# Optimization experiments

Hardware: AMD Instinct MI355X
Metric: run time of the kernel (lower is better)

Reference implementation:

```python
import jax, jax.numpy as jnp
import numpy as np

# Model dims (mamba_ssm defaults for d_model=256)
IN_DIM = 64
D_MODEL = 256
D_INNER = 512      # expand=2
D_STATE = 16
D_CONV = 4
DT_RANK = 16       # ceil(d_model/16)
N_LAYERS = 4
BATCH = 8
SEQ = 1024


def setup_inputs() -> dict:
    key = jax.random.key(0)
    ks = jax.random.split(key, 10)
    s = lambda k, shape, sc: jax.random.normal(k, shape, jnp.float32) * sc
    return {
        "x": jax.random.normal(ks[0], (BATCH, SEQ, IN_DIM), jnp.float32),
        "Wp": s(ks[1], (D_MODEL, IN_DIM), 0.1),
        "bp": jnp.zeros((D_MODEL,), jnp.float32),
        "W_in": s(ks[2], (N_LAYERS, 2 * D_INNER, D_MODEL), 0.05),
        "conv_w": s(ks[3], (N_LAYERS, D_INNER, D_CONV), 0.2),
        "conv_b": jnp.zeros((N_LAYERS, D_INNER), jnp.float32),
        "W_x": s(ks[4], (N_LAYERS, DT_RANK + 2 * D_STATE, D_INNER), 0.05),
        "W_dt": s(ks[5], (N_LAYERS, D_INNER, DT_RANK), 0.1),
        "b_dt": jnp.full((N_LAYERS, D_INNER), -4.6, jnp.float32),  # softplus -> dt ~ 0.01
        "A_log": jnp.log(jnp.broadcast_to(
            jnp.arange(1, D_STATE + 1, dtype=jnp.float32), (N_LAYERS, D_INNER, D_STATE))),
        "Dp": jnp.ones((N_LAYERS, D_INNER), jnp.float32),
        "W_out": s(ks[6], (N_LAYERS, D_MODEL, D_INNER), 0.05),
        "ln_g": jnp.ones((N_LAYERS, D_MODEL), jnp.float32),
        "ln_b": jnp.zeros((N_LAYERS, D_MODEL), jnp.float32),
        "Wf": s(ks[7], (1, D_MODEL), 0.1),
        "bf": jnp.zeros((1,), jnp.float32),
    }


def _layernorm(x, g, b):
    m = x.mean(-1, keepdims=True)
    v = x.var(-1, keepdims=True)
    return (x - m) * jax.lax.rsqrt(v + 1e-5) * g + b


def _mamba(x, W_in, cw, cb, W_x, W_dt, b_dt, A_log, Dp, W_out):
    B, L, _ = x.shape
    xz = jnp.einsum('bld,ed->ble', x, W_in)          # (B,L,2*D_INNER)
    xh, z = jnp.split(xz, 2, axis=-1)
    # causal depthwise conv1d (kernel D_CONV) + silu
    xp = jnp.pad(xh, ((0, 0), (D_CONV - 1, 0), (0, 0)))
    xc = sum(xp[:, k:k + L, :] * cw[:, k] for k in range(D_CONV)) + cb
    xc = jax.nn.silu(xc)
    # input-dependent dt, B, C
    x_dbl = jnp.einsum('bld,ed->ble', xc, W_x)
    dtr = x_dbl[..., :DT_RANK]
    Bm = x_dbl[..., DT_RANK:DT_RANK + D_STATE]       # (B,L,N)
    Cm = x_dbl[..., -D_STATE:]                       # (B,L,N)
    dt = jax.nn.softplus(jnp.einsum('blr,dr->bld', dtr, W_dt) + b_dt)
    A = -jnp.exp(A_log)                              # (D,N)
    dA = jnp.exp(dt[..., None] * A)                  # (B,L,D,N)
    dBu = dt[..., None] * Bm[:, :, None, :] * xc[..., None]
    def step(h, inp):
        dA_t, dBu_t, C_t = inp
        h = dA_t * h + dBu_t                         # (B,D,N)
        return h, jnp.einsum('bdn,bn->bd', h, C_t)
    h0 = jnp.zeros((B, D_INNER, D_STATE), x.dtype)
    _, ys = jax.lax.scan(step, h0, (dA.transpose(1, 0, 2, 3),
                                    dBu.transpose(1, 0, 2, 3),
                                    Cm.transpose(1, 0, 2)))
    y = ys.transpose(1, 0, 2) + Dp * xc              # (B,L,D)
    y = y * jax.nn.silu(z)
    return jnp.einsum('ble,de->bld', y, W_out)


def reference(x, Wp, bp, W_in, conv_w, conv_b, W_x, W_dt, b_dt, A_log, Dp, W_out, ln_g, ln_b, Wf, bf):
    h = jnp.einsum('bli,di->bld', x, Wp) + bp
    for l in range(N_LAYERS):
        y = _mamba(h, W_in[l], conv_w[l], conv_b[l], W_x[l], W_dt[l],
                   b_dt[l], A_log[l], Dp[l], W_out[l])
        h = _layernorm(y, ln_g[l], ln_b[l])          # dropout is identity at eval
    pooled = h.mean(axis=1)                          # AdaptiveAvgPool1d(1) over L
    return pooled @ Wf.T + bf
```

## Files before the change

kernel.cpp:

```cpp
#include <hip/hip_runtime.h>
#include <hip/hip_bf16.h>
#include <math.h>

#define SEQ_LEN 1024
#define BATCH_N 8
#define DMODEL 256
#define DINNER 512
#define DSTATE 16
#define DTRANK 16
#define ROWS (BATCH_N * SEQ_LEN)
#define NCHUNK 64
#define CHUNK (SEQ_LEN / NCHUNK)
#define BD 8

typedef unsigned short u16;
typedef u16 u16x8 __attribute__((ext_vector_type(8)));
typedef short bf16x8 __attribute__((ext_vector_type(8)));
typedef float f32x4 __attribute__((ext_vector_type(4)));

__device__ __forceinline__ float siluf(float x) { return x / (1.f + expf(-x)); }
__device__ __forceinline__ float softplusf(float x) {
    return fmaxf(x, 0.f) + log1pf(expf(-fabsf(x)));
}
__device__ __forceinline__ float fexpf(float x) { return __expf(x); }
__device__ __forceinline__ float softplus_fast(float x) {
    return fmaxf(x, 0.f) + __logf(1.f + __expf(-fabsf(x)));
}
__device__ __forceinline__ float silu_fast(float x) {
    return x * __builtin_amdgcn_rcpf(1.f + __expf(-x));
}
__device__ __forceinline__ u16 bf16_rne(float x) {
    unsigned u = __builtin_bit_cast(unsigned, x);
    return (u16)((u + 0x7FFFu + ((u >> 16) & 1u)) >> 16);
}
__device__ __forceinline__ void cvt_hl(float x, u16& h, u16& l) {
    unsigned u = __builtin_bit_cast(unsigned, x);
    unsigned hb = (u + 0x7FFFu + ((u >> 16) & 1u)) >> 16;
    h = (u16)hb;
    float hf = __builtin_bit_cast(float, hb << 16);
    l = bf16_rne(x - hf);
}
__device__ __forceinline__ float pair_f(u16 h, u16 l) {
    return __builtin_bit_cast(float, (unsigned)h << 16) +
           __builtin_bit_cast(float, (unsigned)l << 16);
}
__device__ __forceinline__ size_t swa(int R, int row, int c) {
    return ((size_t)(c >> 5) * R + row) * 32 + (c & 31);
}

__global__ __launch_bounds__(256) void cvt_x_swz(
    const float* __restrict__ x, u16* __restrict__ dh, u16* __restrict__ dl)
{
    int i = blockIdx.x * 256 + threadIdx.x;
    int row = i >> 6, c = i & 63;
    u16 h, l;
    cvt_hl(x[i], h, l);
    size_t sw = swa(ROWS, row, c);
    dh[sw] = h;
    dl[sw] = l;
}

#define CWT (16384 + 4 * 262144 + 4 * 32768 + 4 * 131072)
__global__ __launch_bounds__(256) void cvt_w_swz(
    const float* __restrict__ Wp, const float* __restrict__ W_in,
    const float* __restrict__ W_x, const float* __restrict__ W_out,
    u16* __restrict__ Wpb, u16* __restrict__ Wib,
    u16* __restrict__ Wxb, u16* __restrict__ Wob)
{
    long i = (long)blockIdx.x * 256 + threadIdx.x;
    if (i >= CWT) return;
    if (i < 16384) {
        int n = (int)(i >> 6), k = (int)(i & 63);
        Wpb[((k >> 5) * 256 + n) * 32 + (k & 31)] = bf16_rne(Wp[n * 64 + k]);
        return;
    }
    i -= 16384;
    if (i < 4 * 262144) {
        int l = (int)(i >> 18), r = (int)(i & 262143);
        int n = r >> 8, k = r & 255;
        Wib[l * 262144 + ((k >> 5) * 1024 + n) * 32 + (k & 31)] =
            bf16_rne(W_in[l * 262144 + n * 256 + k]);
        return;
    }
    i -= 4 * 262144;
    if (i < 4 * 32768) {
        int l = (int)(i >> 15), r = (int)(i & 32767);
        int n = r >> 9, k = r & 511;
        float v = (n < 48) ? W_x[l * 48 * 512 + n * 512 + k] : 0.f;
        Wxb[l * 32768 + ((k >> 5) * 64 + n) * 32 + (k & 31)] = bf16_rne(v);
        return;
    }
    i -= 4 * 32768;
    {
        int l = (int)(i >> 17), r = (int)(i & 131071);
        int n = r >> 9, k = r & 511;
        Wob[l * 131072 + ((k >> 5) * 256 + n) * 32 + (k & 31)] =
            bf16_rne(W_out[l * 131072 + n * 512 + k]);
    }
}

template<int EPI>
__global__ __launch_bounds__(256) void gemm_sw(
    const u16* __restrict__ Ah, const u16* __restrict__ Al,
    const u16* __restrict__ B,
    const float* __restrict__ bias, float* __restrict__ C,
    u16* __restrict__ Ch, u16* __restrict__ Cl,
    int M, int N, int Npad, int K, int ldc)
{
    const int tid  = threadIdx.x;
    const int wave = tid >> 6, lane = tid & 63;
    const int bm   = blockIdx.y * 64, bn = blockIdx.x * 64;
    const int wm   = (wave >> 1) * 32, wn = (wave & 1) * 32;
    const int fr   = lane & 15, quad = lane >> 4;

    f32x4 acc[2][2];
#pragma unroll
    for (int i = 0; i < 2; i++)
#pragma unroll
        for (int j = 0; j < 2; j++) acc[i][j] = (f32x4){0.f, 0.f, 0.f, 0.f};

    const size_t a0 = (size_t)(bm + wm + fr) * 32 + quad * 8;
    const size_t a1 = a0 + 16 * 32;
    const size_t b0 = (size_t)(bn + wn + fr) * 32 + quad * 8;
    const size_t b1 = b0 + 16 * 32;
    const size_t astep = (size_t)M * 32;
    const size_t bstep = (size_t)Npad * 32;

    const u16* pah = Ah;
    const u16* pal = Al;
    const u16* pb  = B;
#pragma unroll 2
    for (int k0 = 0; k0 < K; k0 += 32) {
        bf16x8 ah0 = *(const bf16x8*)(pah + a0);
        bf16x8 ah1 = *(const bf16x8*)(pah + a1);
        bf16x8 al0 = *(const bf16x8*)(pal + a0);
        bf16x8 al1 = *(const bf16x8*)(pal + a1);
        bf16x8 bv0 = *(const bf16x8*)(pb + b0);
        bf16x8 bv1 = *(const bf16x8*)(pb + b1);
        acc[0][0] = __builtin_amdgcn_mfma_f32_16x16x32_bf16(ah0, bv0, acc[0][0], 0, 0, 0);
        acc[0][0] = __builtin_amdgcn_mfma_f32_16x16x32_bf16(al0, bv0, acc[0][0], 0, 0, 0);
        acc[0][1] = __builtin_amdgcn_mfma_f32_16x16x32_bf16(ah0, bv1, acc[0][1], 0, 0, 0);
        acc[0][1] = __builtin_amdgcn_mfma_f32_16x16x32_bf16(al0, bv1, acc[0][1], 0, 0, 0);
        acc[1][0] = __builtin_amdgcn_mfma_f32_16x16x32_bf16(ah1, bv0, acc[1][0], 0, 0, 0);
        acc[1][0] = __builtin_amdgcn_mfma_f32_16x16x32_bf16(al1, bv0, acc[1][0], 0, 0, 0);
        acc[1][1] = __builtin_amdgcn_mfma_f32_16x16x32_bf16(ah1, bv1, acc[1][1], 0, 0, 0);
        acc[1][1] = __builtin_amdgcn_mfma_f32_16x16x32_bf16(al1, bv1, acc[1][1], 0, 0, 0);
        pah += astep; pal += astep; pb += bstep;
    }

#pragma unroll
    for (int i = 0; i < 2; i++) {
        const int r0 = bm + wm + 16 * i + quad * 4;
#pragma unroll
        for (int reg = 0; reg < 4; reg++) {
            const int row = r0 + reg;
#pragma unroll
            for (int j = 0; j < 2; j++) {
                const int col = bn + wn + 16 * j + fr;
                if (col < N) {
                    float v = acc[i][j][reg];
                    if (bias) v += bias[col];
                    if (EPI == 0) {
                        C[(size_t)row * ldc + col] = v;
                    } else {
                        u16 h, l;
                        cvt_hl(v, h, l);
                        size_t sw = swa(M, row, col);
                        Ch[sw] = h;
                        Cl[sw] = l;
                    }
                }
            }
        }
    }
}

__global__ __launch_bounds__(256) void gemm_sw128(
    const u16* __restrict__ Ah, const u16* __restrict__ Al,
    const u16* __restrict__ B, float* __restrict__ C,
    int M, int Npad, int K, int ldc)
{
    const int tid  = threadIdx.x;
    const int wave = tid >> 6, lane = tid & 63;
    const int bm   = blockIdx.y * 64, bn = blockIdx.x * 128;
    const int wm   = (wave >> 1) * 32, wn = (wave & 1) * 64;
    const int fr   = lane & 15, quad = lane >> 4;

    f32x4 acc[2][4];
#pragma unroll
    for (int i = 0; i < 2; i++)
#pragma unroll
        for (int j = 0; j < 4; j++) acc[i][j] = (f32x4){0.f, 0.f, 0.f, 0.f};

    const size_t a0 = (size_t)(bm + wm + fr) * 32 + quad * 8;
    const size_t a1 = a0 + 16 * 32;
    size_t bofs[4];
#pragma unroll
    for (int j = 0; j < 4; j++)
        bofs[j] = (size_t)(bn + wn + 16 * j + fr) * 32 + quad * 8;
    const size_t astep = (size_t)M * 32;
    const size_t bstep = (size_t)Npad * 32;

    const u16* pah = Ah;
    const u16* pal = Al;
    const u16* pb  = B;
    for (int k0 = 0; k0 < K; k0 += 32) {
        bf16x8 ah0 = *(const bf16x8*)(pah + a0);
        bf16x8 ah1 = *(const bf16x8*)(pah + a1);
        bf16x8 al0 = *(const bf16x8*)(pal + a0);
        bf16x8 al1 = *(const bf16x8*)(pal + a1);
        bf16x8 bv[4];
#pragma unroll
        for (int j = 0; j < 4; j++) bv[j] = *(const bf16x8*)(pb + bofs[j]);
#pragma unroll
        for (int j = 0; j < 4; j++) {
            acc[0][j] = __builtin_amdgcn_mfma_f32_16x16x32_bf16(ah0, bv[j], acc[0][j], 0, 0, 0);
            acc[0][j] = __builtin_amdgcn_mfma_f32_16x16x32_bf16(al0, bv[j], acc[0][j], 0, 0, 0);
            acc[1][j] = __builtin_amdgcn_mfma_f32_16x16x32_bf16(ah1, bv[j], acc[1][j], 0, 0, 0);
            acc[1][j] = __builtin_amdgcn_mfma_f32_16x16x32_bf16(al1, bv[j], acc[1][j], 0, 0, 0);
        }
        pah += astep; pal += astep; pb += bstep;
    }

#pragma unroll
    for (int i = 0; i < 2; i++) {
        const int r0 = bm + wm + 16 * i + quad * 4;
#pragma unroll
        for (int reg = 0; reg < 4; reg++) {
            float* crow = C + (size_t)(r0 + reg) * ldc;
#pragma unroll
            for (int j = 0; j < 4; j++)
                crow[bn + wn + 16 * j + fr] = acc[i][j][reg];
        }
    }
}

__global__ __launch_bounds__(256) void conv_silu_k(
    const float* __restrict__ xz, const float* __restrict__ cw,
    const float* __restrict__ cb, u16* __restrict__ xch, u16* __restrict__ xcl)
{
    int idx = blockIdx.x * 256 + threadIdx.x;
    int d = idx & (DINNER - 1);
    int row = idx >> 9;
    int t = row & (SEQ_LEN - 1);
    float4 w = *(const float4*)(cw + d * 4);
    float acc = cb[d];
    const float* p = xz + (size_t)row * 1024 + d;
    if (t >= 3) acc = fmaf(p[-3 * 1024], w.x, acc);
    if (t >= 2) acc = fmaf(p[-2 * 1024], w.y, acc);
    if (t >= 1) acc = fmaf(p[-1 * 1024], w.z, acc);
    acc = fmaf(p[0], w.w, acc);
    float v = siluf(acc);
    u16 h, l;
    cvt_hl(v, h, l);
    size_t sw = swa(ROWS, row, d);
    xch[sw] = h;
    xcl[sw] = l;
}

__global__ __launch_bounds__(512, 4) void scan_k(
    u16* __restrict__ xch,
    u16* __restrict__ xcl,
    const float* __restrict__ xdbl,
    const float* __restrict__ xz,
    const float* __restrict__ A_log,
    const float* __restrict__ Dp,
    const float* __restrict__ Wdt,
    const float* __restrict__ bdt)
{
    const int tid = threadIdx.x;
    const int dl  = tid & (BD - 1);
    const int ch  = tid >> 3;
    const int b   = blockIdx.x & 7;
    const int dg  = blockIdx.x >> 3;
    const int d   = dg * BD + dl;

    __shared__ float ldsS[NCHUNK * BD * 16];
    __shared__ float ldsD[CHUNK * 512];
    __shared__ float ldsT[NCHUNK * BD];

    float wv[16];
#pragma unroll
    for (int i = 0; i < 16; i += 4) *(float4*)&wv[i] = *(const float4*)(Wdt + d * 16 + i);
    const float bb = bdt[d];

    bool pow_ok = true;
#pragma unroll
    for (int n = 0; n < 16; n++) {
        float An = -expf(A_log[d * 16 + n]);
        pow_ok = pow_ok && (fabsf(An + (float)(n + 1)) <= 1e-3f * (float)(n + 1));
    }
    const int t0 = b * SEQ_LEN + ch * CHUNK;
    const int base = (ch * BD + dl) * 16;
    const size_t xcb = ((size_t)(d >> 5) * ROWS) * 32 + (d & 31);

    float S[16];
#pragma unroll
    for (int n = 0; n < 16; n++) S[n] = 0.f;
    float sdt = 0.f;
#pragma unroll 2
    for (int t = 0; t < CHUNK; ++t) {
        const size_t row = (size_t)(t0 + t);
        const float* xr = xdbl + row * 48;
        float qv[16], Bv[16];
#pragma unroll
        for (int i = 0; i < 16; i += 4) *(float4*)&qv[i] = *(const float4*)(xr + i);
#pragma unroll
        for (int i = 0; i < 16; i += 4) *(float4*)&Bv[i] = *(const float4*)(xr + 16 + i);
        float xcv = pair_f(xch[xcb + row * 32], xcl[xcb + row * 32]);
        float s8[8];
#pragma unroll
        for (int i = 0; i < 8; i++) s8[i] = fmaf(qv[i], wv[i], qv[i + 8] * wv[i + 8]);
        float s4_0 = s8[0] + s8[4], s4_1 = s8[1] + s8[5];
        float s4_2 = s8[2] + s8[6], s4_3 = s8[3] + s8[7];
        float dot = bb + ((s4_0 + s4_2) + (s4_1 + s4_3));
        float dtv = softplus_fast(dot);
        ldsD[t * 512 + tid] = dtv;
        sdt += dtv;
        float u = dtv * xcv;
        float p[16];
        if (pow_ok) {
            float e1 = fexpf(-dtv);
            p[0] = e1;
#pragma unroll
            for (int n = 1; n < 8; n++) p[n] = p[n - 1] * e1;
            float e8 = p[7];
#pragma unroll
            for (int n = 8; n < 16; n++) p[n] = p[n - 8] * e8;
        } else {
#pragma unroll
            for (int n = 0; n < 16; n++)
                p[n] = exp2f(dtv * (-expf(A_log[d * 16 + n])) * 1.44269504f);
        }
#pragma unroll
        for (int n = 0; n < 16; n++) S[n] = fmaf(p[n], S[n], u * Bv[n]);
    }
#pragma unroll
    for (int i = 0; i < 16; i += 4) *(float4*)&ldsS[base + i] = *(float4*)&S[i];
    ldsT[tid] = sdt;
    __syncthreads();

    if (tid < BD * 16) {
        const int dd = tid >> 4;
        const int nn = tid & 15;
        const float An = -fexpf(A_log[(dg * BD + dd) * 16 + nn]);
        float h0 = 0.f;
#pragma unroll 4
        for (int c = 0; c < NCHUNK; ++c) {
            const int idx = (c * BD + dd) * 16 + nn;
            float sdtc = ldsT[c * BD + dd];
            float Sv = ldsS[idx];
            float Pv = fexpf(sdtc * An);
            ldsS[idx] = h0;
            h0 = fmaf(Pv, h0, Sv);
        }
    }
    __syncthreads();

    float h[16];
#pragma unroll
    for (int i = 0; i < 16; i += 4) *(float4*)&h[i] = *(float4*)&ldsS[base + i];
    const float Dd = Dp[d];
#pragma unroll 2
    for (int t = 0; t < CHUNK; ++t) {
        const size_t row = (size_t)(t0 + t);
        const float* xr = xdbl + row * 48;
        float Bv[16], Cv[16];
#pragma unroll
        for (int i = 0; i < 16; i += 4) *(float4*)&Bv[i] = *(const float4*)(xr + 16 + i);
#pragma unroll
        for (int i = 0; i < 16; i += 4) *(float4*)&Cv[i] = *(const float4*)(xr + 32 + i);
        float xcv = pair_f(xch[xcb + row * 32], xcl[xcb + row * 32]);
        float zv  = xz[row * 1024 + 512 + d];
        float dtv = ldsD[t * 512 + tid];
        float u = dtv * xcv;
        float p[16];
        if (pow_ok) {
            float e1 = fexpf(-dtv);
            p[0] = e1;
#pragma unroll
            for (int n = 1; n < 8; n++) p[n] = p[n - 1] * e1;
            float e8 = p[7];
#pragma unroll
            for (int n = 8; n < 16; n++) p[n] = p[n - 8] * e8;
        } else {
#pragma unroll
            for (int n = 0; n < 16; n++)
                p[n] = exp2f(dtv * (-expf(A_log[d * 16 + n])) * 1.44269504f);
        }
        float y = 0.f;
#pragma unroll
        for (int n = 0; n < 16; n++) {
            h[n] = fmaf(p[n], h[n], u * Bv[n]);
            y = fmaf(h[n], Cv[n], y);
        }
        y = fmaf(Dd, xcv, y);
        y *= silu_fast(zv);
        u16 yh, yl;
        cvt_hl(y, yh, yl);
        xch[xcb + row * 32] = yh;
        xcl[xcb + row * 32] = yl;
    }
}

__global__ __launch_bounds__(256) void ln_k(
    const float* __restrict__ X, const float* __restrict__ g,
    const float* __restrict__ b2, u16* __restrict__ Yh, u16* __restrict__ Yl)
{
    int lane = threadIdx.x & 63;
    int row = blockIdx.x * 4 + (threadIdx.x >> 6);
    const float4 v = *(const float4*)(X + (size_t)row * 256 + lane * 4);
    float s = v.x + v.y + v.z + v.w;
    float q = v.x * v.x + v.y * v.y + v.z * v.z + v.w * v.w;
#pragma unroll
    for (int o = 1; o < 64; o <<= 1) { s += __shfl_xor(s, o, 64); q += __shfl_xor(q, o, 64); }
    float mean = s * (1.f / 256.f);
    float var = q * (1.f / 256.f) - mean * mean;
    float inv = rsqrtf(var + 1e-5f);
    float4 gg = *(const float4*)(g + lane * 4);
    float4 bb = *(const float4*)(b2 + lane * 4);
    float o0 = (v.x - mean) * inv * gg.x + bb.x;
    float o1 = (v.y - mean) * inv * gg.y + bb.y;
    float o2 = (v.z - mean) * inv * gg.z + bb.z;
    float o3 = (v.w - mean) * inv * gg.w + bb.w;
    ushort4 h4, l4;
    cvt_hl(o0, h4.x, l4.x); cvt_hl(o1, h4.y, l4.y);
    cvt_hl(o2, h4.z, l4.z); cvt_hl(o3, h4.w, l4.w);
    size_t sw = swa(ROWS, row, lane * 4);
    *(ushort4*)(Yh + sw) = h4;
    *(ushort4*)(Yl + sw) = l4;
}

__global__ __launch_bounds__(256) void final1_k(
    const u16* __restrict__ Hh, const u16* __restrict__ Hl,
    const float* __restrict__ Wf, float* __restrict__ part)
{
    const int b   = blockIdx.x >> 6;
    const int ckt = blockIdx.x & 63;
    const int c   = threadIdx.x;
    const size_t cb = ((size_t)(c >> 5) * ROWS) * 32 + (c & 31);
    const int tbase = b * SEQ_LEN + ckt * 16;
    float s = 0.f;
#pragma unroll 4
    for (int t = 0; t < 16; t++) {
        size_t sw = cb + (size_t)(tbase + t) * 32;
        s += pair_f(Hh[sw], Hl[sw]);
    }
    float v = s * Wf[c];
    int lane = c & 63;
#pragma unroll
    for (int o = 1; o < 64; o <<= 1) v += __shfl_xor(v, o, 64);
    __shared__ float red[4];
    if (lane == 0) red[c >> 6] = v;
    __syncthreads();
    if (c == 0) part[blockIdx.x] = red[0] + red[1] + red[2] + red[3];
}

__global__ __launch_bounds__(512) void final2_k(
    const float* __restrict__ part, const float* __restrict__ bf,
    float* __restrict__ out)
{
    int tid = threadIdx.x;
    int b = tid >> 6, i = tid & 63;
    float v = part[b * 64 + i];
#pragma unroll
    for (int o = 1; o < 64; o <<= 1) v += __shfl_xor(v, o, 64);
    if (i == 0) out[b] = v * (1.f / 1024.f) + bf[0];
}

extern "C" void kernel_launch(void* const* d_in, const int* in_sizes, int n_in,
                              void* d_out, int out_size, void* d_ws, size_t ws_size,
                              hipStream_t stream)
{
    const float* x      = (const float*)d_in[0];
    const float* Wp     = (const float*)d_in[1];
    const float* bp     = (const float*)d_in[2];
    const float* W_in   = (const float*)d_in[3];
    const float* conv_w = (const float*)d_in[4];
    const float* conv_b = (const float*)d_in[5];
    const float* W_x    = (const float*)d_in[6];
    const float* W_dt   = (const float*)d_in[7];
    const float* b_dt   = (const float*)d_in[8];
    const float* A_log  = (const float*)d_in[9];
    const float* Dp     = (const float*)d_in[10];
    const float* W_out  = (const float*)d_in[11];
    const float* ln_g   = (const float*)d_in[12];
    const float* ln_b   = (const float*)d_in[13];
    const float* Wf     = (const float*)d_in[14];
    const float* bf     = (const float*)d_in[15];

    char* w = (char*)d_ws;
    float* bufXZ = (float*)w;            w += (size_t)ROWS * 1024 * 4;
    float* bufXD = (float*)w;            w += (size_t)ROWS * 48 * 4;
    u16* xch  = (u16*)w;                 w += (size_t)ROWS * 512 * 2;
    u16* xcl  = (u16*)w;                 w += (size_t)ROWS * 512 * 2;
    u16* hh   = (u16*)w;                 w += (size_t)ROWS * 256 * 2;
    u16* hl   = (u16*)w;                 w += (size_t)ROWS * 256 * 2;
    u16* xih  = (u16*)w;                 w += (size_t)ROWS * 64 * 2;
    u16* xil  = (u16*)w;                 w += (size_t)ROWS * 64 * 2;
    u16* Wpb  = (u16*)w;                 w += (size_t)256 * 64 * 2;
    u16* Wib  = (u16*)w;                 w += (size_t)4 * 1024 * 256 * 2;
    u16* Wxb  = (u16*)w;                 w += (size_t)4 * 64 * 512 * 2;
    u16* Wob  = (u16*)w;                 w += (size_t)4 * 256 * 512 * 2;
    float* part = (float*)w;             w += 512 * 4;
    float* bufO = bufXZ;

    dim3 blk(256);

    cvt_x_swz<<<dim3(ROWS * 64 / 256), blk, 0, stream>>>(x, xih, xil);
    cvt_w_swz<<<dim3((CWT + 255) / 256), blk, 0, stream>>>(
        Wp, W_in, W_x, W_out, Wpb, Wib, Wxb, Wob);

    gemm_sw<1><<<dim3(4, 128), blk, 0, stream>>>(xih, xil, Wpb, bp,
                                                 nullptr, hh, hl,
                                                 ROWS, DMODEL, DMODEL, 64, 0);

    for (int l = 0; l < 4; ++l) {
        const u16* Wil = Wib + (size_t)l * 1024 * 256;
        const u16* Wxl = Wxb + (size_t)l * 64 * 512;
        const u16* Wol = Wob + (size_t)l * 256 * 512;
        const float* cw  = conv_w + (size_t)l * DINNER * 4;
        const float* cb  = conv_b + (size_t)l * DINNER;
        const float* Wdt = W_dt   + (size_t)l * DINNER * DTRANK;
        const float* bdt = b_dt   + (size_t)l * DINNER;
        const float* Al  = A_log  + (size_t)l * DINNER * DSTATE;
        const float* Dl  = Dp     + (size_t)l * DINNER;
        const float* lg  = ln_g   + (size_t)l * DMODEL;
        const float* lb  = ln_b   + (size_t)l * DMODEL;

        gemm_sw128<<<dim3(8, 128), blk, 0, stream>>>(hh, hl, Wil, bufXZ,
                                                     ROWS, 1024, DMODEL, 1024);
        conv_silu_k<<<dim3(ROWS * DINNER / 256), blk, 0, stream>>>(bufXZ, cw, cb, xch, xcl);
        gemm_sw<0><<<dim3(1, 128), blk, 0, stream>>>(xch, xcl, Wxl, nullptr,
                                                     bufXD, nullptr, nullptr,
                                                     ROWS, 48, 64, DINNER, 48);
        scan_k<<<dim3(512), dim3(512), 0, stream>>>(xch, xcl, bufXD, bufXZ,
                                                    Al, Dl, Wdt, bdt);
        gemm_sw<0><<<dim3(4, 128), blk, 0, stream>>>(xch, xcl, Wol, nullptr,
                                                     bufO, nullptr, nullptr,
                                                     ROWS, DMODEL, DMODEL, DINNER, DMODEL);
        ln_k<<<dim3(ROWS / 4), blk, 0, stream>>>(bufO, lg, lb, hh, hl);
    }

    final1_k<<<dim3(512), blk, 0, stream>>>(hh, hl, Wf, part);
    final2_k<<<dim3(1), dim3(512), 0, stream>>>(part, bf, (float*)d_out);

    (void)in_sizes; (void)n_in; (void)out_size; (void)ws_size;
}
```

Baseline: 592.1 us.

## Add dedicated small-N x_dbl GEMM and process four timesteps per thread in conv

New measurement: 539.9 us. 8.8% less time.

```diff
diff --git a/kernel.cpp b/kernel.cpp
--- a/kernel.cpp
+++ b/kernel.cpp
@@ -235,27 +235,84 @@
     }
 }
 
+__global__ __launch_bounds__(256) void gemm_xdbl(
+    const u16* __restrict__ Ah, const u16* __restrict__ Al,
+    const u16* __restrict__ B, float* __restrict__ C)
+{
+    const int tid  = threadIdx.x;
+    const int wave = tid >> 6, lane = tid & 63;
+    const int bm   = blockIdx.x * 32;
+    const int wr   = (wave >> 1) * 16;
+    const int wc   = (wave & 1) * 32;
+    const int fr   = lane & 15, quad = lane >> 4;
+
+    f32x4 acc[2];
+    acc[0] = (f32x4){0.f, 0.f, 0.f, 0.f};
+    acc[1] = (f32x4){0.f, 0.f, 0.f, 0.f};
+
+    const size_t a0 = (size_t)(bm + wr + fr) * 32 + quad * 8;
+    const size_t b0 = (size_t)(wc + fr) * 32 + quad * 8;
+    const size_t b1 = b0 + 16 * 32;
+    const size_t astep = (size_t)ROWS * 32;
+    const size_t bstep = (size_t)64 * 32;
+
+    const u16* pah = Ah;
+    const u16* pal = Al;
+    const u16* pb  = B;
+#pragma unroll 4
+    for (int k0 = 0; k0 < DINNER; k0 += 32) {
+        bf16x8 ah = *(const bf16x8*)(pah + a0);
+        bf16x8 al = *(const bf16x8*)(pal + a0);
+        bf16x8 bv0 = *(const bf16x8*)(pb + b0);
+        bf16x8 bv1 = *(const bf16x8*)(pb + b1);
+        acc[0] = __builtin_amdgcn_mfma_f32_16x16x32_bf16(ah, bv0, acc[0], 0, 0, 0);
+        acc[0] = __builtin_amdgcn_mfma_f32_16x16x32_bf16(al, bv0, acc[0], 0, 0, 0);
+        acc[1] = __builtin_amdgcn_mfma_f32_16x16x32_bf16(ah, bv1, acc[1], 0, 0, 0);
+        acc[1] = __builtin_amdgcn_mfma_f32_16x16x32_bf16(al, bv1, acc[1], 0, 0, 0);
+        pah += astep; pal += astep; pb += bstep;
+    }
+
+    const int r0 = bm + wr + quad * 4;
+#pragma unroll
+    for (int reg = 0; reg < 4; reg++) {
+        const int row = r0 + reg;
+#pragma unroll
+        for (int j = 0; j < 2; j++) {
+            const int col = wc + 16 * j + fr;
+            if (col < 48) C[(size_t)row * 48 + col] = acc[j][reg];
+        }
+    }
+}
+
 __global__ __launch_bounds__(256) void conv_silu_k(
     const float* __restrict__ xz, const float* __restrict__ cw,
     const float* __restrict__ cb, u16* __restrict__ xch, u16* __restrict__ xcl)
 {
     int idx = blockIdx.x * 256 + threadIdx.x;
-    int d = idx & (DINNER - 1);
-    int row = idx >> 9;
-    int t = row & (SEQ_LEN - 1);
+    int d  = idx & (DINNER - 1);
+    int rb = idx >> 9;
+    int row0 = rb * 4;
+    int tb = row0 & (SEQ_LEN - 1);
     float4 w = *(const float4*)(cw + d * 4);
-    float acc = cb[d];
-    const float* p = xz + (size_t)row * 1024 + d;
-    if (t >= 3) acc = fmaf(p[-3 * 1024], w.x, acc);
-    if (t >= 2) acc = fmaf(p[-2 * 1024], w.y, acc);
-    if (t >= 1) acc = fmaf(p[-1 * 1024], w.z, acc);
-    acc = fmaf(p[0], w.w, acc);
-    float v = siluf(acc);
-    u16 h, l;
-    cvt_hl(v, h, l);
-    size_t sw = swa(ROWS, row, d);
-    xch[sw] = h;
-    xcl[sw] = l;
+    const float bbv = cb[d];
+    const float* p = xz + (size_t)row0 * 1024 + d;
+    float xm3 = 0.f, xm2 = 0.f, xm1 = 0.f;
+    if (tb >= 4) { xm3 = p[-3 * 1024]; xm2 = p[-2 * 1024]; xm1 = p[-1 * 1024]; }
+    float x0 = p[0], x1 = p[1024], x2 = p[2 * 1024], x3 = p[3 * 1024];
+    float o[4];
+    float a;
+    a = bbv; a = fmaf(xm3, w.x, a); a = fmaf(xm2, w.y, a); a = fmaf(xm1, w.z, a); a = fmaf(x0, w.w, a); o[0] = a;
+    a = bbv; a = fmaf(xm2, w.x, a); a = fmaf(xm1, w.y, a); a = fmaf(x0, w.z, a);  a = fmaf(x1, w.w, a); o[1] = a;
+    a = bbv; a = fmaf(xm1, w.x, a); a = fmaf(x0, w.y, a);  a = fmaf(x1, w.z, a);  a = fmaf(x2, w.w, a); o[2] = a;
+    a = bbv; a = fmaf(x0, w.x, a);  a = fmaf(x1, w.y, a);  a = fmaf(x2, w.z, a);  a = fmaf(x3, w.w, a); o[3] = a;
+    size_t sw = swa(ROWS, row0, d);
+#pragma unroll
+    for (int i = 0; i < 4; i++) {
+        u16 h, l;
+        cvt_hl(siluf(o[i]), h, l);
+        xch[sw + i * 32] = h;
+        xcl[sw + i * 32] = l;
+    }
 }
 
 __global__ __launch_bounds__(512, 4) void scan_k(
@@ -530,10 +587,9 @@
 
         gemm_sw128<<<dim3(8, 128), blk, 0, stream>>>(hh, hl, Wil, bufXZ,
                                                      ROWS, 1024, DMODEL, 1024);
-        conv_silu_k<<<dim3(ROWS * DINNER / 256), blk, 0, stream>>>(bufXZ, cw, cb, xch, xcl);
-        gemm_sw<0><<<dim3(1, 128), blk, 0, stream>>>(xch, xcl, Wxl, nullptr,
-                                                     bufXD, nullptr, nullptr,
-                                                     ROWS, 48, 64, DINNER, 48);
+        conv_silu_k<<<dim3(ROWS * DINNER / 4 / 256), blk, 0, stream>>>(
+            bufXZ, cw, cb, xch, xcl);
+        gemm_xdbl<<<dim3(ROWS / 32), blk, 0, stream>>>(xch, xcl, Wxl, bufXD);
         scan_k<<<dim3(512), dim3(512), 0, stream>>>(xch, xcl, bufXD, bufXZ,
                                                     Al, Dl, Wdt, bdt);
         gemm_sw<0><<<dim3(4, 128), blk, 0, stream>>>(xch, xcl, Wol, nullptr,
```
